# Kernel tuning notes

Measured on AMD Instinct MI355X. Metric: run time of the kernel, lower is better.

Reference implementation:

```python
import jax, jax.numpy as jnp
import numpy as np

B, C, D, K = 65536, 128, 32, 10
EPS = 1e-12


def setup_inputs() -> dict:
    key = jax.random.key(0)
    k1, k2, k3, k4 = jax.random.split(key, 4)
    data = jax.random.normal(k1, (B, D), dtype=jnp.float32)
    mu = jax.random.normal(k2, (C, D), dtype=jnp.float32)
    # S_inv must be symmetric positive definite (inverse covariance per cluster)
    A = 0.1 * jax.random.normal(k3, (C, D, D), dtype=jnp.float32)
    S_inv = jnp.einsum('cij,ckj->cik', A, A) + jnp.eye(D, dtype=jnp.float32)[None]
    # one-hot class assignment per cluster (int32), as stored in the module
    cls = jax.random.randint(k4, (C,), 0, K)
    cluster_labels = jax.nn.one_hot(cls, K, dtype=jnp.int32)
    return {"data": data, "mu": mu, "S_inv": S_inv, "cluster_labels": cluster_labels}


def reference(data, mu, S_inv, cluster_labels):
    # Mahalanobis distance d2[b,c] = (z_b - mu_c)^T S_inv_c (z_b - mu_c),
    # expanded to avoid a [B, C, D] diff tensor.
    zz = data[:, :, None] * data[:, None, :]            # [B, D, D]
    t1 = jnp.einsum('bde,cde->bc', zz, S_inv)           # z' Sinv z
    Sm = jnp.einsum('cde,ce->cd', S_inv, mu)            # [C, D]
    t2 = data @ Sm.T                                    # z' Sinv mu  [B, C]
    t3 = jnp.einsum('cd,cd->c', mu, Sm)                 # mu' Sinv mu [C]
    d2 = t1 - 2.0 * t2 + t3[None, :]                    # [B, C]
    Gamma = jnp.exp(-0.5 * d2)                          # Gaussian activation
    # defuzzify_batch: normalize activations, project through one-hot labels
    norm_gamma = Gamma / (jnp.sum(Gamma, axis=1, keepdims=True) + EPS)
    label_scores = norm_gamma @ cluster_labels.astype(jnp.float32)  # [B, K]
    preds = jnp.argmax(label_scores, axis=1)
    clusters = jnp.argmax(Gamma, axis=1)
    return label_scores, preds, clusters
```

## Files before the change

kernel.cpp:

```cpp
#include <hip/hip_runtime.h>
#include <cmath>

#define B_N 65536
#define C_N 128
#define D_N 32
#define K_N 10
#define EPS_F 1e-12f
#define SCALE_F (-0.72134752044448169f)

#define NKK 45
#define QFRAG_N (4 * NKK * 64 * 8)

typedef _Float16 f16x8 __attribute__((ext_vector_type(8)));
typedef float    f32x16 __attribute__((ext_vector_type(16)));

static constexpr int WDT[NKK] = {
    0,0,0,0,0,  2,2,2,2,  4,4,4,4,  6,6,6,6,  8,8,8,8,
    10,10,10, 12,12,12, 14,14,14, 16,16,16,
    18,18, 20,20, 22,22, 24,24, 26, 28, 30, 32};
static constexpr int WET[NKK] = {
    0,8,16,24,32,  2,10,18,26,  4,12,20,28,  6,14,22,30,  8,16,24,32,
    10,18,26, 12,20,28, 14,22,30, 16,24,32,
    18,26, 20,28, 22,30, 24,32, 26, 28, 30, 32};

__global__ __launch_bounds__(128) void k_prep(const float* __restrict__ S,
                                              const float* __restrict__ mu,
                                              const int* __restrict__ onehot,
                                              _Float16* __restrict__ Qh,
                                              _Float16* __restrict__ Ql,
                                              int* __restrict__ cls) {
    const int c = blockIdx.x;
    const int tid = threadIdx.x;
    __shared__ float sSm[D_N];
    __shared__ float st3;

    if (tid < D_N) {
        const float* Sr = S + (size_t)c * (D_N * D_N) + (size_t)tid * D_N;
        const float* mr = mu + (size_t)c * D_N;
        float a0 = 0.f, a1 = 0.f;
#pragma unroll
        for (int e = 0; e < D_N; e += 2) {
            a0 = fmaf(Sr[e + 0], mr[e + 0], a0);
            a1 = fmaf(Sr[e + 1], mr[e + 1], a1);
        }
        sSm[tid] = a0 + a1;
    }
    __syncthreads();
    if (tid == 0) {
        const float* mr = mu + (size_t)c * D_N;
        float a = 0.f;
#pragma unroll
        for (int d = 0; d < D_N; ++d) a = fmaf(mr[d], sSm[d], a);
        st3 = a;
        int cl = 0;
#pragma unroll
        for (int k = 0; k < K_N; ++k)
            if (onehot[c * K_N + k] != 0) cl = k;
        cls[c] = cl;
    }
    __syncthreads();

    if (tid < 2 * NKK) {
        const int kk   = tid >> 1;
        const int half = tid & 1;
        const int e0 = WET[kk];
        const int d  = WDT[kk] + half;
        const int ct = c >> 5;
        const size_t base =
            ((size_t)(ct * NKK + kk) * 64 + half * 32 + (c & 31)) * 8;
        const float* Sc = S + (size_t)c * (D_N * D_N);
        for (int j = 0; j < 8; ++j) {
            const int e = e0 + j;
            float q = 0.f;
            if (d <= e && e <= 32) {
                float v;
                if (e < 32)      v = Sc[d * D_N + e] * (d == e ? 1.f : 2.f);
                else if (d < 32) v = -2.f * sSm[d];
                else             v = st3;
                q = SCALE_F * v;
            }
            _Float16 h = (_Float16)q;
            Qh[base + j] = h;
            Ql[base + j] = (_Float16)(q - (float)h);
        }
    }
}

template <int KK>
__device__ __forceinline__ void kstep(const f16x8* __restrict__ QH,
                                      const f16x8* __restrict__ QL,
                                      int lane, bool hi, const float (&y)[34],
                                      f16x8 (&bh)[2][4], f16x8 (&bl)[2][4],
                                      f32x16 (&acc)[4]) {
    constexpr int cur = KK & 1;
    constexpr int nxt = cur ^ 1;
    if constexpr (KK + 1 < NKK) {
#pragma unroll
        for (int ct = 0; ct < 4; ++ct) {
            bh[nxt][ct] = QH[(ct * NKK + KK + 1) * 64 + lane];
            bl[nxt][ct] = QL[(ct * NKK + KK + 1) * 64 + lane];
        }
    }
    constexpr int dA = WDT[KK];
    constexpr int e0 = WET[KK];
    const float yd = hi ? y[dA + 1] : y[dA];
    f16x8 ph, pl;
#pragma unroll
    for (int j = 0; j < 8; ++j) {
        float f = (e0 + j <= 32) ? yd * y[e0 + j] : 0.f;
        _Float16 h = (_Float16)f;
        ph[j] = h;
        pl[j] = (_Float16)(f - (float)h);
    }
#pragma unroll
    for (int ct = 0; ct < 4; ++ct)
        acc[ct] = __builtin_amdgcn_mfma_f32_32x32x16_f16(bh[cur][ct], ph, acc[ct], 0, 0, 0);
#pragma unroll
    for (int ct = 0; ct < 4; ++ct)
        acc[ct] = __builtin_amdgcn_mfma_f32_32x32x16_f16(bl[cur][ct], ph, acc[ct], 0, 0, 0);
#pragma unroll
    for (int ct = 0; ct < 4; ++ct)
        acc[ct] = __builtin_amdgcn_mfma_f32_32x32x16_f16(bh[cur][ct], pl, acc[ct], 0, 0, 0);
}

template <int KK>
__device__ __forceinline__ void loop_from(const f16x8* __restrict__ QH,
                                          const f16x8* __restrict__ QL,
                                          int lane, bool hi, const float (&y)[34],
                                          f16x8 (&bh)[2][4], f16x8 (&bl)[2][4],
                                          f32x16 (&acc)[4]) {
    if constexpr (KK < NKK) {
        kstep<KK>(QH, QL, lane, hi, y, bh, bl, acc);
        loop_from<KK + 1>(QH, QL, lane, hi, y, bh, bl, acc);
    }
}

__global__ __launch_bounds__(256, 2) void k_mainv4(const float* __restrict__ data,
                                                   const _Float16* __restrict__ Qhp,
                                                   const _Float16* __restrict__ Qlp,
                                                   const int* __restrict__ clsp,
                                                   float* __restrict__ out) {
    const int lane = threadIdx.x & 63;
    const int wid  = threadIdx.x >> 6;
    const int b0w  = blockIdx.x * 128 + wid * 32;
    const int col  = lane & 31;
    const bool hi  = lane >= 32;

    __shared__ int lcls[C_N];
    if (threadIdx.x < C_N) lcls[threadIdx.x] = clsp[threadIdx.x];

    float y[34];
    {
        const float4* p0 = (const float4*)(data + (size_t)(b0w + col) * D_N);
#pragma unroll
        for (int i = 0; i < 8; ++i) {
            float4 v = p0[i];
            y[4 * i + 0] = v.x; y[4 * i + 1] = v.y;
            y[4 * i + 2] = v.z; y[4 * i + 3] = v.w;
        }
        y[32] = 1.f; y[33] = 0.f;
    }
    __syncthreads();

    f32x16 acc[4];
#pragma unroll
    for (int ct = 0; ct < 4; ++ct)
#pragma unroll
        for (int g = 0; g < 16; ++g) acc[ct][g] = 0.f;

    const f16x8* QH = (const f16x8*)Qhp;
    const f16x8* QL = (const f16x8*)Qlp;

    f16x8 bh[2][4], bl[2][4];
#pragma unroll
    for (int ct = 0; ct < 4; ++ct) {
        bh[0][ct] = QH[(ct * NKK + 0) * 64 + lane];
        bl[0][ct] = QL[(ct * NKK + 0) * 64 + lane];
    }

    loop_from<0>(QH, QL, lane, hi, y, bh, bl, acc);

    const float hoff = hi ? 4.f : 0.f;
    const int* lc = lcls + (hi ? 4 : 0);
    float sum = 0.f, gmax = -1.f, gcf = 0.f;
    float a0 = 0, a1 = 0, a2 = 0, a3 = 0, a4 = 0, a5 = 0, a6 = 0, a7 = 0, a8 = 0, a9 = 0;
#pragma unroll
    for (int ct = 0; ct < 4; ++ct) {
        float psum = 0.f;
#pragma unroll
        for (int g = 0; g < 16; ++g) {
            float v = acc[ct][g];
            float gm;
            asm("v_exp_f32 %0, %1" : "=v"(gm) : "v"(v));
            const int cbase = ct * 32 + (g & 3) + 8 * (g >> 2);
            int cl = lc[cbase];
            psum += gm;
            float cf = (float)cbase + hoff;
            if (gm > gmax) { gmax = gm; gcf = cf; }
            a0 += (cl == 0) ? gm : 0.f;
            a1 += (cl == 1) ? gm : 0.f;
            a2 += (cl == 2) ? gm : 0.f;
            a3 += (cl == 3) ? gm : 0.f;
            a4 += (cl == 4) ? gm : 0.f;
            a5 += (cl == 5) ? gm : 0.f;
            a6 += (cl == 6) ? gm : 0.f;
            a7 += (cl == 7) ? gm : 0.f;
            a8 += (cl == 8) ? gm : 0.f;
            a9 += (cl == 9) ? gm : 0.f;
        }
        sum += psum;
    }

    sum += __shfl_xor(sum, 32, 64);
    {
        float om = __shfl_xor(gmax, 32, 64);
        float oc = __shfl_xor(gcf, 32, 64);
        bool take = (om > gmax) || (om == gmax && oc < gcf);
        if (take) { gmax = om; gcf = oc; }
    }
    a0 += __shfl_xor(a0, 32, 64);
    a1 += __shfl_xor(a1, 32, 64);
    a2 += __shfl_xor(a2, 32, 64);
    a3 += __shfl_xor(a3, 32, 64);
    a4 += __shfl_xor(a4, 32, 64);
    a5 += __shfl_xor(a5, 32, 64);
    a6 += __shfl_xor(a6, 32, 64);
    a7 += __shfl_xor(a7, 32, 64);
    a8 += __shfl_xor(a8, 32, 64);
    a9 += __shfl_xor(a9, 32, 64);

    if (!hi) {
        const int b = b0w + col;
        float inv = 1.0f / (sum + EPS_F);
        float ls[K_N] = {a0 * inv, a1 * inv, a2 * inv, a3 * inv, a4 * inv,
                         a5 * inv, a6 * inv, a7 * inv, a8 * inv, a9 * inv};
        float best = -1.f;
        int bk = 0;
#pragma unroll
        for (int k = 0; k < K_N; ++k)
            if (ls[k] > best) { best = ls[k]; bk = k; }
        float2* o2 = (float2*)(out + (size_t)b * K_N);
#pragma unroll
        for (int k2 = 0; k2 < K_N / 2; ++k2)
            o2[k2] = make_float2(ls[2 * k2], ls[2 * k2 + 1]);
        out[(size_t)B_N * K_N + b] = (float)bk;
        out[(size_t)B_N * K_N + B_N + b] = gcf;
    }
}

extern "C" void kernel_launch(void* const* d_in, const int* in_sizes, int n_in,
                              void* d_out, int out_size, void* d_ws, size_t ws_size,
                              hipStream_t stream) {
    const float* data   = (const float*)d_in[0];
    const float* mu     = (const float*)d_in[1];
    const float* S      = (const float*)d_in[2];
    const int*   onehot = (const int*)d_in[3];
    float* out = (float*)d_out;

    _Float16* Qh  = (_Float16*)d_ws;
    _Float16* Ql  = Qh + QFRAG_N;
    int*      cls = (int*)(Ql + QFRAG_N);

    hipLaunchKernelGGL(k_prep, dim3(C_N), dim3(128), 0, stream,
                       S, mu, onehot, Qh, Ql, cls);
    hipLaunchKernelGGL(k_mainv4, dim3(B_N / 128), dim3(256), 0, stream,
                       data, Qh, Ql, cls, out);
}
```

Measured before the change: 126.0 us.

## Replace fully unrolled k-step chain with rolled triple-buffered loop using LDS operands

Replaces the compile-time unrolled 45-step MFMA chain with a rolled loop over 48 k-steps that triple-buffers the Q fragment loads. The per-row data vector now lives in shared memory with a padded stride instead of registers. The k-step tile mapping is computed arithmetically rather than taken from constexpr tables. The aim is to cut instruction-cache pressure and register use while keeping global loads in flight ahead of the MFMAs. In exchange it adds LDS reads every step and three extra padded k-steps of MFMA work.

```diff
diff --git a/kernel.cpp b/kernel.cpp
--- a/kernel.cpp
+++ b/kernel.cpp
@@ -8,20 +8,20 @@
 #define EPS_F 1e-12f
 #define SCALE_F (-0.72134752044448169f)
 
-#define NKK 45
+#define NKK 48
 #define QFRAG_N (4 * NKK * 64 * 8)
+#define YSTR 41
 
 typedef _Float16 f16x8 __attribute__((ext_vector_type(8)));
 typedef float    f32x16 __attribute__((ext_vector_type(16)));
 
-static constexpr int WDT[NKK] = {
-    0,0,0,0,0,  2,2,2,2,  4,4,4,4,  6,6,6,6,  8,8,8,8,
-    10,10,10, 12,12,12, 14,14,14, 16,16,16,
-    18,18, 20,20, 22,22, 24,24, 26, 28, 30, 32};
-static constexpr int WET[NKK] = {
-    0,8,16,24,32,  2,10,18,26,  4,12,20,28,  6,14,22,30,  8,16,24,32,
-    10,18,26, 12,20,28, 14,22,30, 16,24,32,
-    18,26, 20,28, 22,30, 24,32, 26, 28, 30, 32};
+__device__ __forceinline__ void mdkk(int kk, int& dA, int& e0) {
+    int w = (kk >= 17) + (kk >= 30) + (kk >= 39) + (kk >= 44);
+    int off = w == 0 ? 0 : (w == 1 ? 17 : (w == 2 ? 30 : (w == 3 ? 39 : 44)));
+    int r = kk - off;
+    dA = 2 * r;
+    e0 = 2 * r + 8 * w;
+}
 
 __global__ __launch_bounds__(128) void k_prep(const float* __restrict__ S,
                                               const float* __restrict__ mu,
@@ -63,8 +63,9 @@
     if (tid < 2 * NKK) {
         const int kk   = tid >> 1;
         const int half = tid & 1;
-        const int e0 = WET[kk];
-        const int d  = WDT[kk] + half;
+        int dA, e0;
+        mdkk(kk, dA, e0);
+        const int d  = dA + half;
         const int ct = c >> 5;
         const size_t base =
             ((size_t)(ct * NKK + kk) * 64 + half * 32 + (c & 31)) * 8;
@@ -86,79 +87,79 @@
     }
 }
 
-template <int KK>
-__device__ __forceinline__ void kstep(const f16x8* __restrict__ QH,
-                                      const f16x8* __restrict__ QL,
-                                      int lane, bool hi, const float (&y)[34],
-                                      f16x8 (&bh)[2][4], f16x8 (&bl)[2][4],
-                                      f32x16 (&acc)[4]) {
-    constexpr int cur = KK & 1;
-    constexpr int nxt = cur ^ 1;
-    if constexpr (KK + 1 < NKK) {
-#pragma unroll
-        for (int ct = 0; ct < 4; ++ct) {
-            bh[nxt][ct] = QH[(ct * NKK + KK + 1) * 64 + lane];
-            bl[nxt][ct] = QL[(ct * NKK + KK + 1) * 64 + lane];
-        }
-    }
-    constexpr int dA = WDT[KK];
-    constexpr int e0 = WET[KK];
-    const float yd = hi ? y[dA + 1] : y[dA];
+__device__ __forceinline__ void ldq(const f16x8* __restrict__ QH,
+                                    const f16x8* __restrict__ QL,
+                                    int kk, int lane,
+                                    f16x8 (&qh)[4], f16x8 (&ql)[4]) {
+#pragma unroll
+    for (int ct = 0; ct < 4; ++ct) {
+        qh[ct] = QH[(ct * NKK + kk) * 64 + lane];
+        ql[ct] = QL[(ct * NKK + kk) * 64 + lane];
+    }
+}
+
+__device__ __forceinline__ void ldy(const float* sy, int ybase, int hioff,
+                                    int kk, float& yd, float (&yw)[8]) {
+    int dA, e0;
+    mdkk(kk, dA, e0);
+    yd = sy[ybase + dA + hioff];
+#pragma unroll
+    for (int j = 0; j < 8; ++j) yw[j] = sy[ybase + e0 + j];
+}
+
+__device__ __forceinline__ void domfma(const f16x8 (&qh)[4], const f16x8 (&ql)[4],
+                                       float yd, const float (&yw)[8],
+                                       f32x16 (&acc)[4]) {
     f16x8 ph, pl;
 #pragma unroll
     for (int j = 0; j < 8; ++j) {
-        float f = (e0 + j <= 32) ? yd * y[e0 + j] : 0.f;
+        float f = yd * yw[j];
         _Float16 h = (_Float16)f;
         ph[j] = h;
         pl[j] = (_Float16)(f - (float)h);
     }
 #pragma unroll
     for (int ct = 0; ct < 4; ++ct)
-        acc[ct] = __builtin_amdgcn_mfma_f32_32x32x16_f16(bh[cur][ct], ph, acc[ct], 0, 0, 0);
-#pragma unroll
-    for (int ct = 0; ct < 4; ++ct)
-        acc[ct] = __builtin_amdgcn_mfma_f32_32x32x16_f16(bl[cur][ct], ph, acc[ct], 0, 0, 0);
-#pragma unroll
-    for (int ct = 0; ct < 4; ++ct)
-        acc[ct] = __builtin_amdgcn_mfma_f32_32x32x16_f16(bh[cur][ct], pl, acc[ct], 0, 0, 0);
-}
-
-template <int KK>
-__device__ __forceinline__ void loop_from(const f16x8* __restrict__ QH,
-                                          const f16x8* __restrict__ QL,
-                                          int lane, bool hi, const float (&y)[34],
-                                          f16x8 (&bh)[2][4], f16x8 (&bl)[2][4],
-                                          f32x16 (&acc)[4]) {
-    if constexpr (KK < NKK) {
-        kstep<KK>(QH, QL, lane, hi, y, bh, bl, acc);
-        loop_from<KK + 1>(QH, QL, lane, hi, y, bh, bl, acc);
-    }
-}
-
-__global__ __launch_bounds__(256, 2) void k_mainv4(const float* __restrict__ data,
+        acc[ct] = __builtin_amdgcn_mfma_f32_32x32x16_f16(qh[ct], ph, acc[ct], 0, 0, 0);
+#pragma unroll
+    for (int ct = 0; ct < 4; ++ct)
+        acc[ct] = __builtin_amdgcn_mfma_f32_32x32x16_f16(ql[ct], ph, acc[ct], 0, 0, 0);
+#pragma unroll
+    for (int ct = 0; ct < 4; ++ct)
+        acc[ct] = __builtin_amdgcn_mfma_f32_32x32x16_f16(qh[ct], pl, acc[ct], 0, 0, 0);
+}
+
+__global__ __launch_bounds__(256, 2) void k_mainv5(const float* __restrict__ data,
                                                    const _Float16* __restrict__ Qhp,
                                                    const _Float16* __restrict__ Qlp,
                                                    const int* __restrict__ clsp,
                                                    float* __restrict__ out) {
-    const int lane = threadIdx.x & 63;
-    const int wid  = threadIdx.x >> 6;
+    const int tid  = threadIdx.x;
+    const int lane = tid & 63;
+    const int wid  = tid >> 6;
     const int b0w  = blockIdx.x * 128 + wid * 32;
     const int col  = lane & 31;
     const bool hi  = lane >= 32;
 
+    __shared__ float sy[256 * YSTR + 64];
     __shared__ int lcls[C_N];
-    if (threadIdx.x < C_N) lcls[threadIdx.x] = clsp[threadIdx.x];
-
-    float y[34];
+    if (tid < C_N) lcls[tid] = clsp[tid];
+
+    const int ybase = tid * YSTR;
     {
         const float4* p0 = (const float4*)(data + (size_t)(b0w + col) * D_N);
 #pragma unroll
         for (int i = 0; i < 8; ++i) {
             float4 v = p0[i];
-            y[4 * i + 0] = v.x; y[4 * i + 1] = v.y;
-            y[4 * i + 2] = v.z; y[4 * i + 3] = v.w;
-        }
-        y[32] = 1.f; y[33] = 0.f;
+            sy[ybase + 4 * i + 0] = v.x;
+            sy[ybase + 4 * i + 1] = v.y;
+            sy[ybase + 4 * i + 2] = v.z;
+            sy[ybase + 4 * i + 3] = v.w;
+        }
+        sy[ybase + 32] = 1.f;
+#pragma unroll
+        for (int i = 33; i < YSTR; ++i) sy[ybase + i] = 0.f;
+        if (tid < 64) sy[256 * YSTR + tid] = 0.f;
     }
     __syncthreads();
 
@@ -170,15 +171,32 @@
 
     const f16x8* QH = (const f16x8*)Qhp;
     const f16x8* QL = (const f16x8*)Qlp;
-
-    f16x8 bh[2][4], bl[2][4];
-#pragma unroll
-    for (int ct = 0; ct < 4; ++ct) {
-        bh[0][ct] = QH[(ct * NKK + 0) * 64 + lane];
-        bl[0][ct] = QL[(ct * NKK + 0) * 64 + lane];
-    }
-
-    loop_from<0>(QH, QL, lane, hi, y, bh, bl, acc);
+    const int hioff = hi ? 1 : 0;
+
+    f16x8 qhA[4], qlA[4], qhB[4], qlB[4], qhC[4], qlC[4];
+    float ydA, ywA[8], ydB, ywB[8], ydC, ywC[8];
+
+    ldq(QH, QL, 0, lane, qhA, qlA);
+    ldq(QH, QL, 1, lane, qhB, qlB);
+    ldq(QH, QL, 2, lane, qhC, qlC);
+    ldy(sy, ybase, hioff, 0, ydA, ywA);
+
+#pragma clang loop unroll(disable)
+    for (int kk = 0; kk < NKK; kk += 3) {
+        ldy(sy, ybase, hioff, kk + 1, ydB, ywB);
+        domfma(qhA, qlA, ydA, ywA, acc);
+        { int t = kk + 3 < NKK ? kk + 3 : NKK - 1;
+          ldq(QH, QL, t, lane, qhA, qlA); }
+        ldy(sy, ybase, hioff, kk + 2, ydC, ywC);
+        domfma(qhB, qlB, ydB, ywB, acc);
+        { int t = kk + 4 < NKK ? kk + 4 : NKK - 1;
+          ldq(QH, QL, t, lane, qhB, qlB); }
+        { int t = kk + 3 < NKK ? kk + 3 : NKK - 1;
+          ldy(sy, ybase, hioff, t, ydA, ywA); }
+        domfma(qhC, qlC, ydC, ywC, acc);
+        { int t = kk + 5 < NKK ? kk + 5 : NKK - 1;
+          ldq(QH, QL, t, lane, qhC, qlC); }
+    }
 
     const float hoff = hi ? 4.f : 0.f;
     const int* lc = lcls + (hi ? 4 : 0);
@@ -263,6 +281,6 @@
 
     hipLaunchKernelGGL(k_prep, dim3(C_N), dim3(128), 0, stream,
                        S, mu, onehot, Qh, Ql, cls);
-    hipLaunchKernelGGL(k_mainv4, dim3(B_N / 128), dim3(256), 0, stream,
+    hipLaunchKernelGGL(k_mainv5, dim3(B_N / 128), dim3(256), 0, stream,
                        data, Qh, Ql, cls, out);
 }
```

Result: faster. 114.3 us (-9.3%).
